# Kernel optimization log

Measured on AMD Instinct MI355X. Metric: run time of the kernel, lower is better.

## Reference

```python
import jax, jax.numpy as jnp
import numpy as np

N = 50000      # nodes (batched molecular graphs)
E = 800000     # edges
G = 2048       # graphs in the batch
IN = 128       # in_channels
H = 128        # hidden
EPS = 1e-5     # BatchNorm eps


def _glorot(key, shape):
    lim = float(np.sqrt(6.0 / (shape[0] + shape[1])))
    return jax.random.uniform(key, shape, jnp.float32, -lim, lim)


def setup_inputs() -> dict:
    key = jax.random.key(0)
    ks = jax.random.split(key, 8)
    x = jax.random.normal(ks[0], (N, IN), jnp.float32)
    edge_index = jax.random.randint(ks[1], (2, E), 0, N, dtype=jnp.int64)
    batch = jnp.sort(jax.random.randint(ks[2], (N,), 0, G, dtype=jnp.int64))
    return {
        "x": x,
        "edge_index": edge_index,
        "batch": batch,
        "W1": _glorot(ks[3], (IN, H)), "b1": jnp.zeros((H,), jnp.float32),
        "gamma1": jnp.ones((H,), jnp.float32), "beta1": jnp.zeros((H,), jnp.float32),
        "W2": _glorot(ks[4], (H, H)), "b2": jnp.zeros((H,), jnp.float32),
        "gamma2": jnp.ones((H,), jnp.float32), "beta2": jnp.zeros((H,), jnp.float32),
        "Wout": _glorot(ks[5], (H, 1)), "bout": jnp.zeros((1,), jnp.float32),
    }


def gcn_conv(x, src, dst, W, b):
    # PyG GCNConv: add self-loops, symmetric norm D^-1/2 (A+I) D^-1/2, transform-first.
    n = x.shape[0]
    loop = jnp.arange(n, dtype=src.dtype)
    s = jnp.concatenate([src, loop])           # [E+N]
    d = jnp.concatenate([dst, loop])
    deg = jax.ops.segment_sum(jnp.ones_like(d, jnp.float32), d, num_segments=n)
    dinv = jnp.where(deg > 0, jax.lax.rsqrt(deg), 0.0)
    norm = dinv[s] * dinv[d]                   # [E+N]
    xw = x @ W                                 # [N, H] transform first (cheaper)
    msg = xw[s] * norm[:, None]                # [E+N, H] gathered, normalized messages
    out = jax.ops.segment_sum(msg, d, num_segments=n)  # scatter-add aggregate
    return out + b


def batch_norm(x, gamma, beta):
    # BatchNorm1d training-mode forward: batch stats, biased variance.
    mean = jnp.mean(x, axis=0)
    var = jnp.mean(jnp.square(x - mean), axis=0)
    return (x - mean) * jax.lax.rsqrt(var + EPS) * gamma + beta


def reference(x, edge_index, batch, W1, b1, gamma1, beta1, W2, b2, gamma2, beta2, Wout, bout):
    src, dst = edge_index[0], edge_index[1]
    h = jax.nn.relu(batch_norm(gcn_conv(x, src, dst, W1, b1), gamma1, beta1))
    h = jax.nn.relu(batch_norm(gcn_conv(h, src, dst, W2, b2), gamma2, beta2))
    # global_mean_pool over graph ids
    sums = jax.ops.segment_sum(h, batch, num_segments=G)            # [G, H]
    cnts = jax.ops.segment_sum(jnp.ones((h.shape[0],), h.dtype), batch, num_segments=G)
    pooled = sums / jnp.maximum(cnts, 1.0)[:, None]
    return pooled @ Wout + bout                                     # [G, 1]
```

## Files before the change

kernel.cpp:

```cpp
#include <hip/hip_runtime.h>
#include <stdint.h>

#define HD 128
#define EPS 1e-5f
#define NPB 256
#define SENT 0xFFFFFFFFu

typedef __attribute__((ext_vector_type(8))) short bf16x8;
typedef __attribute__((ext_vector_type(4))) float f32x4;

__device__ inline unsigned bf_round(float f) {
  unsigned u = __float_as_uint(f);
  return (u + 0x7fffu + ((u >> 16) & 1u)) >> 16;
}
__device__ inline float2 bf_unpack2(unsigned u) {
  float2 r;
  r.x = __uint_as_float(u << 16);
  r.y = __uint_as_float(u & 0xffff0000u);
  return r;
}

__global__ __launch_bounds__(256) void k_phaseA(const int* __restrict__ src, const int* __restrict__ dst,
                                                int* __restrict__ bline, unsigned* __restrict__ arena,
                                                int E, int NBKT, int capLines, int chunk) {
  __shared__ int hist[NPB], gbase[NPB], ccap[NPB], lpos[NPB];
  const int t = threadIdx.x;
  for (int i = t; i < NPB; i += 256) { hist[i] = 0; lpos[i] = 0; }
  __syncthreads();
  const int e0 = blockIdx.x * chunk;
  const int e1 = (e0 + chunk < E) ? e0 + chunk : E;
  for (int i = e0 + t; i < e1; i += 256) atomicAdd(&hist[dst[i] >> 8], 1);
  __syncthreads();
  for (int b = t; b < NBKT; b += 256) {
    int n = hist[b];
    int nl = (n + 15) >> 4;
    int base = nl ? atomicAdd(&bline[b * 16], nl) : 0;
    if (base + nl > capLines) nl = (base < capLines) ? capLines - base : 0;
    gbase[b] = b * capLines * 16 + base * 16;
    ccap[b] = nl * 16;
  }
  __syncthreads();
  for (int i = e0 + t; i < e1; i += 256) {
    int d = dst[i];
    int b = d >> 8;
    int lp = atomicAdd(&lpos[b], 1);
    if (lp < ccap[b]) arena[gbase[b] + lp] = ((unsigned)src[i] << 8) | (unsigned)(d & 255);
  }
  __syncthreads();
  for (int b = t; b < NBKT; b += 256) {
    int n = lpos[b] < ccap[b] ? lpos[b] : ccap[b];
    for (int j = n; j < ccap[b]; ++j) arena[gbase[b] + j] = SENT;
  }
}

__global__ __launch_bounds__(256) void k_phaseB(const unsigned* __restrict__ arena,
                                                const int* __restrict__ bline,
                                                unsigned short* __restrict__ colidx,
                                                unsigned* __restrict__ nodeinfo,
                                                float* __restrict__ dinv,
                                                int N, int capLines) {
  __shared__ int deg[NPB], pos[NPB], scan[NPB];
  const int b = blockIdx.x;
  const int t = threadIdx.x;
  deg[t] = 0;
  __syncthreads();
  int used = bline[b * 16];
  if (used > capLines) used = capLines;
  const int slots = used * 16;
  const unsigned* seg = arena + (size_t)b * capLines * 16;
  for (int s = t; s < slots; s += 256) {
    unsigned u = seg[s];
    if (u != SENT) atomicAdd(&deg[u & 255], 1);
  }
  __syncthreads();
  int v = deg[t];
  scan[t] = v;
  __syncthreads();
  for (int off = 1; off < 256; off <<= 1) {
    int tv = (t >= off) ? scan[t - off] : 0;
    __syncthreads();
    scan[t] += tv;
    __syncthreads();
  }
  int prefix = scan[t] - v;
  pos[t] = prefix;
  int n = b * NPB + t;
  if (n < N) {
    unsigned off = (unsigned)(b * capLines * 16 + prefix);
    unsigned d8 = (unsigned)(v < 255 ? v : 255);
    nodeinfo[n] = (off << 8) | d8;
    dinv[n] = rsqrtf((float)v + 1.0f);
  }
  __syncthreads();
  unsigned short* cseg = colidx + (size_t)b * capLines * 16;
  for (int s = t; s < slots; s += 256) {
    unsigned u = seg[s];
    if (u != SENT) {
      int p = atomicAdd(&pos[u & 255], 1);
      cseg[p] = (unsigned short)(u >> 8);
    }
  }
}

#define SAB_LD 136
__global__ __launch_bounds__(256) void k_gemm(const float* __restrict__ A, const float* __restrict__ W,
                                              unsigned* __restrict__ Yp, int N,
                                              const float* __restrict__ dinv,
                                              const float* __restrict__ scale,
                                              const float* __restrict__ shift) {
  __shared__ unsigned short sWt[128 * SAB_LD];
  __shared__ unsigned short sAb[64 * SAB_LD];
  const int tid = threadIdx.x;
  const int row0 = blockIdx.x * 64;
  for (int i = tid * 4; i < 128 * 128; i += 256 * 4) {
    int k = i >> 7, c = i & 127;
    float4 v = *(const float4*)&W[i];
    sWt[(c + 0) * SAB_LD + k] = (unsigned short)bf_round(v.x);
    sWt[(c + 1) * SAB_LD + k] = (unsigned short)bf_round(v.y);
    sWt[(c + 2) * SAB_LD + k] = (unsigned short)bf_round(v.z);
    sWt[(c + 3) * SAB_LD + k] = (unsigned short)bf_round(v.w);
  }
  for (int i = tid * 4; i < 64 * 128; i += 256 * 4) {
    int r = i >> 7, c = i & 127;
    int gr = row0 + r;
    float4 v = make_float4(0.f, 0.f, 0.f, 0.f);
    if (gr < N) v = *(const float4*)&A[(size_t)gr * HD + c];
    if (scale) {
      v.x = fmaxf(0.f, v.x * scale[c + 0] + shift[c + 0]);
      v.y = fmaxf(0.f, v.y * scale[c + 1] + shift[c + 1]);
      v.z = fmaxf(0.f, v.z * scale[c + 2] + shift[c + 2]);
      v.w = fmaxf(0.f, v.w * scale[c + 3] + shift[c + 3]);
    }
    unsigned lo = bf_round(v.x) | (bf_round(v.y) << 16);
    unsigned hi = bf_round(v.z) | (bf_round(v.w) << 16);
    *(uint2*)&sAb[r * SAB_LD + c] = make_uint2(lo, hi);
  }
  __syncthreads();
  const int w = tid >> 6;
  const int l = tid & 63;
  const int lr = l & 15;
  const int lk = (l >> 4) * 8;
  const unsigned short* aRow = &sAb[(w * 16 + lr) * SAB_LD];
  f32x4 acc[8];
#pragma unroll
  for (int t = 0; t < 8; ++t) acc[t] = (f32x4){0.f, 0.f, 0.f, 0.f};
#pragma unroll
  for (int kk = 0; kk < 128; kk += 32) {
    bf16x8 af = *(const bf16x8*)&aRow[kk + lk];
#pragma unroll
    for (int t = 0; t < 8; ++t) {
      bf16x8 bfr = *(const bf16x8*)&sWt[(t * 16 + lr) * SAB_LD + kk + lk];
      acc[t] = __builtin_amdgcn_mfma_f32_16x16x32_bf16(af, bfr, acc[t], 0, 0, 0);
    }
  }
  const int rbase = row0 + w * 16 + (l >> 4) * 4;
#pragma unroll
  for (int j = 0; j < 4; ++j) {
    int r = rbase + j;
    float d = (r < N) ? dinv[r] : 0.f;
#pragma unroll
    for (int t = 0; t < 8; ++t) {
      float v = acc[t][j] * d;
      float vn = __shfl_xor(v, 1, 64);
      if ((lr & 1) == 0 && r < N) {
        Yp[(size_t)r * 64 + t * 8 + (lr >> 1)] = bf_round(v) | (bf_round(vn) << 16);
      }
    }
  }
}

__global__ __launch_bounds__(256) void k_aggregate(const unsigned* __restrict__ Yp,
                                                   const unsigned* __restrict__ nodeinfo,
                                                   const unsigned short* __restrict__ colidx,
                                                   const float* __restrict__ dinv,
                                                   float* __restrict__ Out, int N) {
  int n = (blockIdx.x * blockDim.x + threadIdx.x) >> 6;
  int lane = threadIdx.x & 63;
  if (n >= N) return;
  const unsigned info = nodeinfo[n];
  const int beg = (int)(info >> 8);
  const int deg = (int)(info & 255);
  const int m = deg < 64 ? deg : 64;
  int nbr = (lane < deg) ? (int)colidx[beg + lane] : 0;
  float2 self = bf_unpack2(Yp[(size_t)n * 64 + lane]);
  float ax = self.x, ay = self.y;
  int j = 0;
  for (; j + 8 <= m; j += 8) {
    unsigned u0 = Yp[(size_t)__shfl(nbr, j + 0, 64) * 64 + lane];
    unsigned u1 = Yp[(size_t)__shfl(nbr, j + 1, 64) * 64 + lane];
    unsigned u2 = Yp[(size_t)__shfl(nbr, j + 2, 64) * 64 + lane];
    unsigned u3 = Yp[(size_t)__shfl(nbr, j + 3, 64) * 64 + lane];
    unsigned u4 = Yp[(size_t)__shfl(nbr, j + 4, 64) * 64 + lane];
    unsigned u5 = Yp[(size_t)__shfl(nbr, j + 5, 64) * 64 + lane];
    unsigned u6 = Yp[(size_t)__shfl(nbr, j + 6, 64) * 64 + lane];
    unsigned u7 = Yp[(size_t)__shfl(nbr, j + 7, 64) * 64 + lane];
    float2 v0 = bf_unpack2(u0), v1 = bf_unpack2(u1), v2 = bf_unpack2(u2), v3 = bf_unpack2(u3);
    float2 v4 = bf_unpack2(u4), v5 = bf_unpack2(u5), v6 = bf_unpack2(u6), v7 = bf_unpack2(u7);
    ax += ((v0.x + v1.x) + (v2.x + v3.x)) + ((v4.x + v5.x) + (v6.x + v7.x));
    ay += ((v0.y + v1.y) + (v2.y + v3.y)) + ((v4.y + v5.y) + (v6.y + v7.y));
  }
  for (; j < m; ++j) {
    float2 v0 = bf_unpack2(Yp[(size_t)__shfl(nbr, j, 64) * 64 + lane]);
    ax += v0.x; ay += v0.y;
  }
  for (int e = beg + 64; e < beg + deg; ++e) {
    float2 v0 = bf_unpack2(Yp[(size_t)colidx[e] * 64 + lane]);
    ax += v0.x; ay += v0.y;
  }
  float dd = dinv[n];
  float2 o; o.x = ax * dd; o.y = ay * dd;
  *(float2*)&Out[(size_t)n * HD + lane * 2] = o;
}

__global__ __launch_bounds__(256) void k_colstats(const float* __restrict__ X, int N,
                                                  float* __restrict__ sums) {
  const int c = threadIdx.x & 127;
  const int half = threadIdx.x >> 7;
  float s = 0.f, q = 0.f;
  for (int r = blockIdx.x * 2 + half; r < N; r += gridDim.x * 2) {
    float v = X[(size_t)r * HD + c];
    s += v; q += v * v;
  }
  __shared__ float ls[256], lq[256];
  ls[threadIdx.x] = s; lq[threadIdx.x] = q;
  __syncthreads();
  if (threadIdx.x < 128) {
    atomicAdd(&sums[c], ls[threadIdx.x] + ls[threadIdx.x + 128]);
    atomicAdd(&sums[128 + c], lq[threadIdx.x] + lq[threadIdx.x + 128]);
  }
}

__global__ void k_bnparams(const float* __restrict__ sums, float invN,
                           const float* __restrict__ gamma, const float* __restrict__ beta,
                           float* __restrict__ scale, float* __restrict__ shift) {
  int c = threadIdx.x;
  if (c < HD) {
    float mean = sums[c] * invN;
    float var = sums[HD + c] * invN - mean * mean;
    float sc = gamma[c] * rsqrtf(var + EPS);
    scale[c] = sc;
    shift[c] = beta[c] - mean * sc;
  }
}

__global__ __launch_bounds__(256) void k_finalnode(const float* __restrict__ Agg,
                                                   const float* __restrict__ scale,
                                                   const float* __restrict__ shift,
                                                   const float* __restrict__ wout,
                                                   const int* __restrict__ batch,
                                                   float* __restrict__ gsum, int N) {
  int n = (blockIdx.x * blockDim.x + threadIdx.x) >> 6;
  int lane = threadIdx.x & 63;
  if (n >= N) return;
  int c = lane * 2;
  float2 v = *(const float2*)&Agg[(size_t)n * HD + c];
  float h0 = fmaxf(0.f, v.x * scale[c] + shift[c]);
  float h1 = fmaxf(0.f, v.y * scale[c + 1] + shift[c + 1]);
  float p = h0 * wout[c] + h1 * wout[c + 1];
  for (int off = 32; off > 0; off >>= 1) p += __shfl_down(p, off);
  if (lane == 0) atomicAdd(&gsum[batch[n]], p);
}

__global__ void k_finalout(const float* __restrict__ gsum, const int* __restrict__ batch,
                           const float* __restrict__ bout, float* __restrict__ out,
                           int G, int N) {
  int g = blockIdx.x * blockDim.x + threadIdx.x;
  if (g >= G) return;
  int lo = 0, hi = N;
  while (lo < hi) { int mid = (lo + hi) >> 1; if (batch[mid] < g) lo = mid + 1; else hi = mid; }
  int lb = lo;
  hi = N;
  while (lo < hi) { int mid = (lo + hi) >> 1; if (batch[mid] <= g) lo = mid + 1; else hi = mid; }
  float cnt = (float)(lo - lb);
  out[g] = gsum[g] / fmaxf(cnt, 1.0f) + bout[0];
}

extern "C" void kernel_launch(void* const* d_in, const int* in_sizes, int n_in,
                              void* d_out, int out_size, void* d_ws, size_t ws_size,
                              hipStream_t stream) {
  (void)n_in; (void)ws_size;
  const float* x      = (const float*)d_in[0];
  const int*   ei     = (const int*)d_in[1];
  const int*   batch  = (const int*)d_in[2];
  const float* W1     = (const float*)d_in[3];
  const float* gamma1 = (const float*)d_in[5];
  const float* beta1  = (const float*)d_in[6];
  const float* W2     = (const float*)d_in[7];
  const float* gamma2 = (const float*)d_in[9];
  const float* beta2  = (const float*)d_in[10];
  const float* wout   = (const float*)d_in[11];
  const float* bout   = (const float*)d_in[12];
  float* out = (float*)d_out;

  const int N = in_sizes[0] / HD;
  const int E = in_sizes[1] / 2;
  const int G = out_size;
  const int* src = ei;
  const int* dst = ei + E;
  const int NBKT = (N + NPB - 1) / NPB;
  const int NWGA = 128;
  const int chunk = (E + NWGA - 1) / NWGA;
  const int capLines = E / (NBKT * 16) + NWGA / 2 + 96;
  const int capSlots = capLines * 16;

  char* p = (char*)d_ws;
  auto carve = [&](size_t bytes) { char* r = p; p += (bytes + 255) & ~(size_t)255; return r; };
  unsigned* bufY = (unsigned*)carve((size_t)N * 64 * 4);
  float* bufAgg  = (float*)carve((size_t)N * HD * 4);
  unsigned* arena = (unsigned*)carve((size_t)NBKT * capSlots * 4);
  unsigned short* colidx = (unsigned short*)carve((size_t)NBKT * capSlots * 2);
  unsigned* nodeinfo = (unsigned*)carve((size_t)N * 4);
  float* dinv    = (float*)carve((size_t)N * 4);
  float* scale1  = (float*)carve(HD * 4);
  float* shift1  = (float*)carve(HD * 4);
  float* scale2  = (float*)carve(HD * 4);
  float* shift2  = (float*)carve(HD * 4);
  char* z0 = p;
  int*   bline = (int*)carve((size_t)NBKT * 16 * 4);
  float* sums1 = (float*)carve(256 * 4);
  float* sums2 = (float*)carve(256 * 4);
  float* gsum  = (float*)carve((size_t)G * 4);
  size_t zbytes = (size_t)(p - z0);

  hipMemsetAsync(z0, 0, zbytes, stream);

  k_phaseA<<<NWGA, 256, 0, stream>>>(src, dst, bline, arena, E, NBKT, capLines, chunk);
  k_phaseB<<<NBKT, 256, 0, stream>>>(arena, bline, colidx, nodeinfo, dinv, N, capLines);

  int gblocks = (N + 63) / 64;
  int ablocks = (N + 3) / 4;
  k_gemm<<<gblocks, 256, 0, stream>>>(x, W1, bufY, N, dinv, nullptr, nullptr);
  k_aggregate<<<ablocks, 256, 0, stream>>>(bufY, nodeinfo, colidx, dinv, bufAgg, N);
  k_colstats<<<512, 256, 0, stream>>>(bufAgg, N, sums1);
  k_bnparams<<<1, 128, 0, stream>>>(sums1, 1.0f / (float)N, gamma1, beta1, scale1, shift1);
  k_gemm<<<gblocks, 256, 0, stream>>>(bufAgg, W2, bufY, N, dinv, scale1, shift1);
  k_aggregate<<<ablocks, 256, 0, stream>>>(bufY, nodeinfo, colidx, dinv, bufAgg, N);
  k_colstats<<<512, 256, 0, stream>>>(bufAgg, N, sums2);
  k_bnparams<<<1, 128, 0, stream>>>(sums2, 1.0f / (float)N, gamma2, beta2, scale2, shift2);
  k_finalnode<<<ablocks, 256, 0, stream>>>(bufAgg, scale2, shift2, wout, batch, gsum, N);
  k_finalout<<<(G + 255) / 256, 256, 0, stream>>>(gsum, batch, bout, out, G, N);
}
```

Before: 260.3 us.

## Store aggregated features in bf16 and replace pooling atomics with per-graph segment sums

The aggregation output buffer changes from fp32 to packed bf16, halving the bytes written by aggregate and read by colstats, the second GEMM and the final node kernel. Colstats is reworked to read packed pairs. The final pooling no longer does per-node atomicAdd into graph sums: it writes a per-node scalar, and each graph thread sums its contiguous range. The hipMemsetAsync is replaced by a small zeroing kernel. Risk: BatchNorm statistics are now computed from bf16-rounded values, which adds precision error.

```diff
diff --git a/kernel.cpp b/kernel.cpp
--- a/kernel.cpp
+++ b/kernel.cpp
@@ -12,12 +12,22 @@
 __device__ inline unsigned bf_round(float f) {
   unsigned u = __float_as_uint(f);
   return (u + 0x7fffu + ((u >> 16) & 1u)) >> 16;
+}
+__device__ inline unsigned bf_pack2(float x, float y) {
+  return bf_round(x) | (bf_round(y) << 16);
 }
 __device__ inline float2 bf_unpack2(unsigned u) {
   float2 r;
   r.x = __uint_as_float(u << 16);
   r.y = __uint_as_float(u & 0xffff0000u);
   return r;
+}
+
+__global__ void k_zero(int* __restrict__ bline, float* __restrict__ sums1,
+                       float* __restrict__ sums2, int nbline) {
+  int i = blockIdx.x * 256 + threadIdx.x;
+  if (i < nbline) bline[i] = 0;
+  if (i < 256) { sums1[i] = 0.f; sums2[i] = 0.f; }
 }
 
 __global__ __launch_bounds__(256) void k_phaseA(const int* __restrict__ src, const int* __restrict__ dst,
@@ -103,7 +113,9 @@
 }
 
 #define SAB_LD 136
-__global__ __launch_bounds__(256) void k_gemm(const float* __restrict__ A, const float* __restrict__ W,
+__global__ __launch_bounds__(256) void k_gemm(const float* __restrict__ Af32,
+                                              const unsigned* __restrict__ Abf,
+                                              const float* __restrict__ W,
                                               unsigned* __restrict__ Yp, int N,
                                               const float* __restrict__ dinv,
                                               const float* __restrict__ scale,
@@ -124,7 +136,15 @@
     int r = i >> 7, c = i & 127;
     int gr = row0 + r;
     float4 v = make_float4(0.f, 0.f, 0.f, 0.f);
-    if (gr < N) v = *(const float4*)&A[(size_t)gr * HD + c];
+    if (gr < N) {
+      if (Abf) {
+        uint2 u = *(const uint2*)&Abf[(size_t)gr * 64 + (c >> 1)];
+        float2 a = bf_unpack2(u.x), bq = bf_unpack2(u.y);
+        v = make_float4(a.x, a.y, bq.x, bq.y);
+      } else {
+        v = *(const float4*)&Af32[(size_t)gr * HD + c];
+      }
+    }
     if (scale) {
       v.x = fmaxf(0.f, v.x * scale[c + 0] + shift[c + 0]);
       v.y = fmaxf(0.f, v.y * scale[c + 1] + shift[c + 1]);
@@ -173,7 +193,7 @@
                                                    const unsigned* __restrict__ nodeinfo,
                                                    const unsigned short* __restrict__ colidx,
                                                    const float* __restrict__ dinv,
-                                                   float* __restrict__ Out, int N) {
+                                                   unsigned* __restrict__ Out, int N) {
   int n = (blockIdx.x * blockDim.x + threadIdx.x) >> 6;
   int lane = threadIdx.x & 63;
   if (n >= N) return;
@@ -208,25 +228,32 @@
     ax += v0.x; ay += v0.y;
   }
   float dd = dinv[n];
-  float2 o; o.x = ax * dd; o.y = ay * dd;
-  *(float2*)&Out[(size_t)n * HD + lane * 2] = o;
-}
-
-__global__ __launch_bounds__(256) void k_colstats(const float* __restrict__ X, int N,
+  Out[(size_t)n * 64 + lane] = bf_pack2(ax * dd, ay * dd);
+}
+
+__global__ __launch_bounds__(256) void k_colstats(const unsigned* __restrict__ X, int N,
                                                   float* __restrict__ sums) {
-  const int c = threadIdx.x & 127;
-  const int half = threadIdx.x >> 7;
-  float s = 0.f, q = 0.f;
-  for (int r = blockIdx.x * 2 + half; r < N; r += gridDim.x * 2) {
-    float v = X[(size_t)r * HD + c];
-    s += v; q += v * v;
-  }
-  __shared__ float ls[256], lq[256];
-  ls[threadIdx.x] = s; lq[threadIdx.x] = q;
-  __syncthreads();
-  if (threadIdx.x < 128) {
-    atomicAdd(&sums[c], ls[threadIdx.x] + ls[threadIdx.x + 128]);
-    atomicAdd(&sums[128 + c], lq[threadIdx.x] + lq[threadIdx.x + 128]);
+  const int c2 = threadIdx.x & 63;
+  const int half = threadIdx.x >> 6;
+  float sx = 0.f, sy = 0.f, qx = 0.f, qy = 0.f;
+  for (int r = blockIdx.x * 4 + half; r < N; r += gridDim.x * 4) {
+    float2 v = bf_unpack2(X[(size_t)r * 64 + c2]);
+    sx += v.x; sy += v.y; qx += v.x * v.x; qy += v.y * v.y;
+  }
+  __shared__ float l0[256], l1[256], l2[256], l3[256];
+  l0[threadIdx.x] = sx; l1[threadIdx.x] = sy; l2[threadIdx.x] = qx; l3[threadIdx.x] = qy;
+  __syncthreads();
+  if (threadIdx.x < 64) {
+    int t = threadIdx.x;
+    sx = l0[t] + l0[t + 64] + l0[t + 128] + l0[t + 192];
+    sy = l1[t] + l1[t + 64] + l1[t + 128] + l1[t + 192];
+    qx = l2[t] + l2[t + 64] + l2[t + 128] + l2[t + 192];
+    qy = l3[t] + l3[t + 64] + l3[t + 128] + l3[t + 192];
+    int c = t * 2;
+    atomicAdd(&sums[c], sx);
+    atomicAdd(&sums[c + 1], sy);
+    atomicAdd(&sums[128 + c], qx);
+    atomicAdd(&sums[129 + c], qy);
   }
 }
 
@@ -243,25 +270,24 @@
   }
 }
 
-__global__ __launch_bounds__(256) void k_finalnode(const float* __restrict__ Agg,
+__global__ __launch_bounds__(256) void k_finalnode(const unsigned* __restrict__ Agg,
                                                    const float* __restrict__ scale,
                                                    const float* __restrict__ shift,
                                                    const float* __restrict__ wout,
-                                                   const int* __restrict__ batch,
-                                                   float* __restrict__ gsum, int N) {
+                                                   float* __restrict__ nodescalar, int N) {
   int n = (blockIdx.x * blockDim.x + threadIdx.x) >> 6;
   int lane = threadIdx.x & 63;
   if (n >= N) return;
   int c = lane * 2;
-  float2 v = *(const float2*)&Agg[(size_t)n * HD + c];
+  float2 v = bf_unpack2(Agg[(size_t)n * 64 + lane]);
   float h0 = fmaxf(0.f, v.x * scale[c] + shift[c]);
   float h1 = fmaxf(0.f, v.y * scale[c + 1] + shift[c + 1]);
   float p = h0 * wout[c] + h1 * wout[c + 1];
   for (int off = 32; off > 0; off >>= 1) p += __shfl_down(p, off);
-  if (lane == 0) atomicAdd(&gsum[batch[n]], p);
-}
-
-__global__ void k_finalout(const float* __restrict__ gsum, const int* __restrict__ batch,
+  if (lane == 0) nodescalar[n] = p;
+}
+
+__global__ void k_finalout(const float* __restrict__ nodescalar, const int* __restrict__ batch,
                            const float* __restrict__ bout, float* __restrict__ out,
                            int G, int N) {
   int g = blockIdx.x * blockDim.x + threadIdx.x;
@@ -271,8 +297,10 @@
   int lb = lo;
   hi = N;
   while (lo < hi) { int mid = (lo + hi) >> 1; if (batch[mid] <= g) lo = mid + 1; else hi = mid; }
+  float s = 0.f;
+  for (int i = lb; i < lo; ++i) s += nodescalar[i];
   float cnt = (float)(lo - lb);
-  out[g] = gsum[g] / fmaxf(cnt, 1.0f) + bout[0];
+  out[g] = s / fmaxf(cnt, 1.0f) + bout[0];
 }
 
 extern "C" void kernel_launch(void* const* d_in, const int* in_sizes, int n_in,
@@ -306,37 +334,37 @@
   char* p = (char*)d_ws;
   auto carve = [&](size_t bytes) { char* r = p; p += (bytes + 255) & ~(size_t)255; return r; };
   unsigned* bufY = (unsigned*)carve((size_t)N * 64 * 4);
-  float* bufAgg  = (float*)carve((size_t)N * HD * 4);
+  unsigned* bufAgg = (unsigned*)carve((size_t)N * 64 * 4);
   unsigned* arena = (unsigned*)carve((size_t)NBKT * capSlots * 4);
   unsigned short* colidx = (unsigned short*)carve((size_t)NBKT * capSlots * 2);
   unsigned* nodeinfo = (unsigned*)carve((size_t)N * 4);
   float* dinv    = (float*)carve((size_t)N * 4);
+  float* nodescalar = (float*)carve((size_t)N * 4);
   float* scale1  = (float*)carve(HD * 4);
   float* shift1  = (float*)carve(HD * 4);
   float* scale2  = (float*)carve(HD * 4);
   float* shift2  = (float*)carve(HD * 4);
-  char* z0 = p;
   int*   bline = (int*)carve((size_t)NBKT * 16 * 4);
   float* sums1 = (float*)carve(256 * 4);
   float* sums2 = (float*)carve(256 * 4);
-  float* gsum  = (float*)carve((size_t)G * 4);
-  size_t zbytes = (size_t)(p - z0);
-
-  hipMemsetAsync(z0, 0, zbytes, stream);
+
+  const int nbline = NBKT * 16;
+  int zblocks = (nbline + 255) / 256;
+  k_zero<<<zblocks, 256, 0, stream>>>(bline, sums1, sums2, nbline);
 
   k_phaseA<<<NWGA, 256, 0, stream>>>(src, dst, bline, arena, E, NBKT, capLines, chunk);
   k_phaseB<<<NBKT, 256, 0, stream>>>(arena, bline, colidx, nodeinfo, dinv, N, capLines);
 
   int gblocks = (N + 63) / 64;
   int ablocks = (N + 3) / 4;
-  k_gemm<<<gblocks, 256, 0, stream>>>(x, W1, bufY, N, dinv, nullptr, nullptr);
+  k_gemm<<<gblocks, 256, 0, stream>>>(x, nullptr, W1, bufY, N, dinv, nullptr, nullptr);
   k_aggregate<<<ablocks, 256, 0, stream>>>(bufY, nodeinfo, colidx, dinv, bufAgg, N);
   k_colstats<<<512, 256, 0, stream>>>(bufAgg, N, sums1);
   k_bnparams<<<1, 128, 0, stream>>>(sums1, 1.0f / (float)N, gamma1, beta1, scale1, shift1);
-  k_gemm<<<gblocks, 256, 0, stream>>>(bufAgg, W2, bufY, N, dinv, scale1, shift1);
+  k_gemm<<<gblocks, 256, 0, stream>>>(nullptr, bufAgg, W2, bufY, N, dinv, scale1, shift1);
   k_aggregate<<<ablocks, 256, 0, stream>>>(bufY, nodeinfo, colidx, dinv, bufAgg, N);
   k_colstats<<<512, 256, 0, stream>>>(bufAgg, N, sums2);
   k_bnparams<<<1, 128, 0, stream>>>(sums2, 1.0f / (float)N, gamma2, beta2, scale2, shift2);
-  k_finalnode<<<ablocks, 256, 0, stream>>>(bufAgg, scale2, shift2, wout, batch, gsum, N);
-  k_finalout<<<(G + 255) / 256, 256, 0, stream>>>(gsum, batch, bout, out, G, N);
-}
+  k_finalnode<<<ablocks, 256, 0, stream>>>(bufAgg, scale2, shift2, wout, nodescalar, N);
+  k_finalout<<<(G + 255) / 256, 256, 0, stream>>>(nodescalar, batch, bout, out, G, N);
+}
```

Result: no change. 257.3 us (-1.1%).
